# Kernel tuning notes

Hardware: AMD Instinct MI355X
Metric: run time of the kernel (lower is better)

Reference implementation:

```python
import jax, jax.numpy as jnp
import numpy as np

NUM_LAYERS, D_IN, D_M, D_S, D_D, K = 4, 768, 1536, 16, 96, 4
EPS = 1e-6


def rmsnorm(x, w):
    return x * jax.lax.rsqrt(jnp.mean(x * x, axis=-1, keepdims=True) + EPS) * w


def depthwise_causal_conv(x, w, b):
    # x: [B, D_M, L], w: [D_M, K], b: [D_M]
    # torch Conv1d with padding=K-1 followed by [..., :L] == causal left-pad conv
    xp = jnp.pad(x, ((0, 0), (0, 0), (K - 1, 0)))
    y = jax.lax.conv_general_dilated(
        xp, w[:, None, :], (1,), 'VALID',
        dimension_numbers=('NCH', 'OIH', 'NCH'),
        feature_group_count=D_M)
    return y + b[None, :, None]


def mamba_block(seq, in_w, out_w, sB, sC, sD0, sD1w, sD1b, cw, cb, A_log, Dp):
    ab = seq @ in_w.T                       # [B,L,2*D_M]
    a, bgate = ab[..., :D_M], ab[..., D_M:]
    x = jnp.swapaxes(a, 1, 2)               # [B,D_M,L]
    a = jnp.swapaxes(depthwise_causal_conv(x, cw, cb), 1, 2)
    a = jax.nn.silu(a)
    # --- selective SSM ---
    A = -jnp.exp(A_log)                     # [D_M,D_S]
    Bm = a @ sB.T                           # [B,L,D_S]
    Cm = a @ sC.T                           # [B,L,D_S]
    delta = jax.nn.softplus((a @ sD0.T) @ sD1w.T + sD1b)  # [B,L,D_M]
    A_bar = jnp.exp(delta[..., None] * A)   # [B,L,D_M,D_S]
    X_bar = delta[..., None] * Bm[:, :, None, :] * a[..., None]

    def step(h, AX):
        At, Xt = AX                         # [B,D_M,D_S]
        h = At * h + Xt
        return h, h

    h0 = jnp.zeros((seq.shape[0], D_M, D_S), seq.dtype)
    _, hs = jax.lax.scan(step, h0, (jnp.swapaxes(A_bar, 0, 1), jnp.swapaxes(X_bar, 0, 1)))
    hid = jnp.swapaxes(hs, 0, 1)            # [B,L,D_M,D_S]
    out = jnp.einsum('blds,bls->bld', hid, Cm) + Dp * a
    out = out * jax.nn.silu(bgate)
    return out @ out_w.T


def setup_inputs() -> dict:
    key = jax.random.key(0)
    ks = jax.random.split(key, 16)
    s = 0.02
    tok = jax.random.randint(ks[0], (2, 1024), 0, 32000)
    embedding = jax.random.normal(ks[1], (32000, D_IN), jnp.float32) * s
    in_proj_w = jax.random.normal(ks[2], (NUM_LAYERS, 2 * D_M, D_IN), jnp.float32) * (D_IN ** -0.5)
    out_proj_w = jax.random.normal(ks[3], (NUM_LAYERS, D_IN, D_M), jnp.float32) * (D_M ** -0.5)
    sB_w = jax.random.normal(ks[4], (NUM_LAYERS, D_S, D_M), jnp.float32) * (D_M ** -0.5)
    sC_w = jax.random.normal(ks[5], (NUM_LAYERS, D_S, D_M), jnp.float32) * (D_M ** -0.5)
    sD0_w = jax.random.normal(ks[6], (NUM_LAYERS, D_D, D_M), jnp.float32) * (D_M ** -0.5)
    sD1_w = jax.random.uniform(ks[7], (NUM_LAYERS, D_M, D_D), jnp.float32, -(D_D ** -0.5), D_D ** -0.5)
    # dt-bias init exactly as in the module
    u = jax.random.uniform(ks[8], (NUM_LAYERS, D_M), jnp.float32)
    dt = jnp.clip(jnp.exp(u * (np.log(0.1) - np.log(0.001)) + np.log(0.001)), 1e-4, None)
    sD1_b = dt + jnp.log(-jnp.expm1(-dt))
    conv_w = jax.random.normal(ks[9], (NUM_LAYERS, D_M, K), jnp.float32) * (K ** -0.5)
    conv_b = jnp.zeros((NUM_LAYERS, D_M), jnp.float32)
    A_log = jnp.broadcast_to(jnp.log(jnp.arange(1, D_S + 1, dtype=jnp.float32)), (NUM_LAYERS, D_M, D_S))
    D = jnp.ones((NUM_LAYERS, D_M), jnp.float32)
    norm_w = jnp.ones((NUM_LAYERS, D_IN), jnp.float32)
    norm_f_w = jnp.ones((D_IN,), jnp.float32)
    head_w = jax.random.normal(ks[10], (32000, D_IN), jnp.float32) * (D_IN ** -0.5)
    return dict(tok=tok, embedding=embedding, in_proj_w=in_proj_w, out_proj_w=out_proj_w,
                sB_w=sB_w, sC_w=sC_w, sD0_w=sD0_w, sD1_w=sD1_w, sD1_b=sD1_b,
                conv_w=conv_w, conv_b=conv_b, A_log=A_log, D=D,
                norm_w=norm_w, norm_f_w=norm_f_w, head_w=head_w)


def reference(tok, embedding, in_proj_w, out_proj_w, sB_w, sC_w, sD0_w, sD1_w, sD1_b,
              conv_w, conv_b, A_log, D, norm_w, norm_f_w, head_w):
    seq = embedding[tok]                    # [B,L,D_IN]
    for i in range(NUM_LAYERS):
        seq = mamba_block(rmsnorm(seq, norm_w[i]),
                          in_proj_w[i], out_proj_w[i], sB_w[i], sC_w[i],
                          sD0_w[i], sD1_w[i], sD1_b[i], conv_w[i], conv_b[i],
                          A_log[i], D[i]) + seq
    seq = rmsnorm(seq, norm_f_w)
    return seq @ head_w.T                   # [B,L,vocab]
```

## Files before the change

kernel.cpp:

```cpp
#include <hip/hip_runtime.h>
#include <math.h>

#define BATCH 2
#define SEQLEN 1024
#define NTOK 2048
#define DIN 768
#define DM 1536
#define DS 16
#define DD 96
#define EPS 1e-6f
#define NC 64
#define CL 16
#define NG (BATCH*DM*DS)

typedef __attribute__((ext_vector_type(8))) short short8;
typedef __attribute__((ext_vector_type(4))) float f32x4;

static __device__ __forceinline__ unsigned short f2bf(float f) {
    unsigned int u = __float_as_uint(f);
    u += 0x7fff + ((u >> 16) & 1);
    return (unsigned short)(u >> 16);
}

__global__ __launch_bounds__(192) void embed_kernel(const int* __restrict__ tok,
                                                    const float* __restrict__ emb,
                                                    float* __restrict__ seq) {
    int m = blockIdx.x;
    int t = tok[m];
    const float4* src = (const float4*)(emb + (size_t)t * DIN);
    float4* dst = (float4*)(seq + (size_t)m * DIN);
    dst[threadIdx.x] = src[threadIdx.x];
}

__global__ __launch_bounds__(256) void zero_kernel(float* __restrict__ p, int n4) {
    int i = blockIdx.x * 256 + threadIdx.x;
    if (i < n4) ((float4*)p)[i] = make_float4(0.f, 0.f, 0.f, 0.f);
}

__global__ __launch_bounds__(256) void wcat_kernel(const float* __restrict__ sB,
                                                   const float* __restrict__ sC,
                                                   const float* __restrict__ sD0,
                                                   unsigned short* __restrict__ out) {
    int idx = blockIdx.x * 256 + threadIdx.x;
    int k = idx % DM;
    int row = (idx / DM) & 127;
    int layer = idx / (DM * 128);
    float v;
    if (row < 16)      v = sB[((size_t)layer * 16 + row) * DM + k];
    else if (row < 32) v = sC[((size_t)layer * 16 + (row - 16)) * DM + k];
    else               v = sD0[((size_t)layer * 96 + (row - 32)) * DM + k];
    out[idx] = f2bf(v);
}

__global__ __launch_bounds__(256) void rmsnorm_kernel(const float* __restrict__ in,
                                                      const float* __restrict__ w,
                                                      unsigned short* __restrict__ out) {
    int m = blockIdx.x;
    const float* x = in + (size_t)m * DIN;
    float v[3];
    float s = 0.f;
#pragma unroll
    for (int j = 0; j < 3; j++) {
        v[j] = x[threadIdx.x + 256 * j];
        s += v[j] * v[j];
    }
#pragma unroll
    for (int off = 32; off; off >>= 1) s += __shfl_down(s, off);
    __shared__ float wsum[4];
    int lane = threadIdx.x & 63, wv = threadIdx.x >> 6;
    if (lane == 0) wsum[wv] = s;
    __syncthreads();
    float tot = wsum[0] + wsum[1] + wsum[2] + wsum[3];
    float scale = rsqrtf(tot / (float)DIN + EPS);
#pragma unroll
    for (int j = 0; j < 3; j++) {
        int c = threadIdx.x + 256 * j;
        out[(size_t)m * DIN + c] = f2bf(v[j] * scale * w[c]);
    }
}

template <int EPI, int BSRC, int KSPLIT, int XCDSWZ>
__global__ __launch_bounds__(256) void gemm_mfma(const unsigned short* __restrict__ A,
                                                 const void* __restrict__ Bv,
                                                 float* __restrict__ C, int N, int K, int nbx) {
    __shared__ unsigned short As[128 * 32];
    __shared__ unsigned short Bs[128 * 32];
    int tid = threadIdx.x;
    int lane = tid & 63, w = tid >> 6;
    int wm = w >> 1, wn = w & 1;
    int fm = lane & 15, fk = lane >> 4;

    int bx, by;
    if (XCDSWZ) {
        int lin = blockIdx.y * gridDim.x + blockIdx.x;
        int q = gridDim.x >> 3;
        int x = lin & 7;
        int t = lin >> 3;
        by = t % gridDim.y;
        bx = x * q + t / gridDim.y;
        if (bx >= nbx) return;
    } else {
        bx = blockIdx.x; by = blockIdx.y;
    }

    const unsigned short* Ab   = A + (size_t)by * 128 * K;
    const unsigned short* Bb16 = (const unsigned short*)Bv + (size_t)bx * 128 * K;
    const float*          Bb32 = (const float*)Bv + (size_t)bx * 128 * K;
    int r0 = tid >> 2;
    int ko = (tid & 3) * 8;
    const float* Bp = Bb32 + (size_t)(tid >> 1) * K + (tid & 1) * 16;

    int kchunk = K / KSPLIT;
    int kbeg = (KSPLIT > 1) ? blockIdx.z * kchunk : 0;
    int kend = kbeg + kchunk;

    f32x4 acc[4][4];
#pragma unroll
    for (int i = 0; i < 4; i++)
#pragma unroll
        for (int j = 0; j < 4; j++) acc[i][j] = (f32x4){0.f, 0.f, 0.f, 0.f};

    float4 bc0, bc1, bc2, bc3;
    unsigned short *bdst0 = nullptr, *bdst1 = nullptr;
    if (BSRC == 1) {
        int r = tid >> 1;
        int sz = (r >> 1) & 3;
        int d0 = (tid & 1) * 2;
        bdst0 = Bs + r * 32 + ((d0 + 0) ^ sz) * 8;
        bdst1 = Bs + r * 32 + ((d0 + 1) ^ sz) * 8;
        bc0 = *(const float4*)(Bp + kbeg);
        bc1 = *(const float4*)(Bp + kbeg + 4);
        bc2 = *(const float4*)(Bp + kbeg + 8);
        bc3 = *(const float4*)(Bp + kbeg + 12);
    }

    for (int k0 = kbeg; k0 < kend; k0 += 32) {
        __syncthreads();
        if (BSRC == 1) {
            short8 p0, p1;
            p0[0] = (short)f2bf(bc0.x); p0[1] = (short)f2bf(bc0.y);
            p0[2] = (short)f2bf(bc0.z); p0[3] = (short)f2bf(bc0.w);
            p0[4] = (short)f2bf(bc1.x); p0[5] = (short)f2bf(bc1.y);
            p0[6] = (short)f2bf(bc1.z); p0[7] = (short)f2bf(bc1.w);
            p1[0] = (short)f2bf(bc2.x); p1[1] = (short)f2bf(bc2.y);
            p1[2] = (short)f2bf(bc2.z); p1[3] = (short)f2bf(bc2.w);
            p1[4] = (short)f2bf(bc3.x); p1[5] = (short)f2bf(bc3.y);
            p1[6] = (short)f2bf(bc3.z); p1[7] = (short)f2bf(bc3.w);
            *(short8*)bdst0 = p0;
            *(short8*)bdst1 = p1;
        }
#pragma unroll
        for (int j = 0; j < 2; j++) {
            int row = r0 + j * 64;
            int c = tid + j * 256;
            __builtin_amdgcn_global_load_lds(
                (const __attribute__((address_space(1))) unsigned int*)(const void*)(Ab + (size_t)row * K + k0 + ko),
                (__attribute__((address_space(3))) unsigned int*)(void*)(As + c * 8), 16, 0, 0);
            if (BSRC == 0)
                __builtin_amdgcn_global_load_lds(
                    (const __attribute__((address_space(1))) unsigned int*)(const void*)(Bb16 + (size_t)row * K + k0 + ko),
                    (__attribute__((address_space(3))) unsigned int*)(void*)(Bs + c * 8), 16, 0, 0);
        }
        __syncthreads();

        if (BSRC == 1) {
            int kn = (k0 + 32 < kend) ? (k0 + 32) : kbeg;
            bc0 = *(const float4*)(Bp + kn);
            bc1 = *(const float4*)(Bp + kn + 4);
            bc2 = *(const float4*)(Bp + kn + 8);
            bc3 = *(const float4*)(Bp + kn + 12);
        }

        short8 af[4], bfv[4];
#pragma unroll
        for (int i = 0; i < 4; i++)
            af[i] = *(const short8*)(As + (wm * 64 + i * 16 + fm) * 32 + fk * 8);
#pragma unroll
        for (int j = 0; j < 4; j++) {
            int R = wn * 64 + j * 16 + fm;
            int dswz = (BSRC == 1) ? (fk ^ ((R >> 1) & 3)) : fk;
            bfv[j] = *(const short8*)(Bs + R * 32 + dswz * 8);
        }
#pragma unroll
        for (int i = 0; i < 4; i++)
#pragma unroll
            for (int j = 0; j < 4; j++)
                acc[i][j] = __builtin_amdgcn_mfma_f32_16x16x32_bf16(af[i], bfv[j], acc[i][j], 0, 0, 0);
    }

    int rowb = by * 128 + wm * 64;
    int colb = bx * 128 + wn * 64;
#pragma unroll
    for (int i = 0; i < 4; i++)
#pragma unroll
        for (int j = 0; j < 4; j++)
#pragma unroll
            for (int r = 0; r < 4; r++) {
                int row = rowb + i * 16 + fk * 4 + r;
                int col = colb + j * 16 + fm;
                size_t off = (size_t)row * N + col;
                if (EPI == 0)      C[off] = acc[i][j][r];
                else if (EPI == 1) C[off] += acc[i][j][r];
                else               unsafeAtomicAdd(&C[off], acc[i][j][r]);
            }
}

__global__ __launch_bounds__(256) void conv_silu_kernel(const float* __restrict__ ab,
                                                        const float* __restrict__ cw,
                                                        const float* __restrict__ cb,
                                                        float* __restrict__ out,
                                                        unsigned short* __restrict__ outb) {
    int idx = blockIdx.x * 256 + threadIdx.x;
    int c = idx % DM;
    int t = idx / DM;
    int l = t % SEQLEN;
    float4 w4 = ((const float4*)cw)[c];
    float y = cb[c];
    y = fmaf(w4.w, ab[(size_t)t * (2 * DM) + c], y);
    if (l >= 1) y = fmaf(w4.z, ab[(size_t)(t - 1) * (2 * DM) + c], y);
    if (l >= 2) y = fmaf(w4.y, ab[(size_t)(t - 2) * (2 * DM) + c], y);
    if (l >= 3) y = fmaf(w4.x, ab[(size_t)(t - 3) * (2 * DM) + c], y);
    float sv = y / (1.f + expf(-y));
    out[(size_t)t * DM + c] = sv;
    outb[(size_t)t * DM + c] = f2bf(sv);
}

__global__ __launch_bounds__(256) void gemm32_softplus(const float* __restrict__ A, int lda,
                                                       const float* __restrict__ B,
                                                       float* __restrict__ C, int N, int K,
                                                       const float* __restrict__ bias) {
    __shared__ float As[16][68];
    __shared__ float Bs[16][68];
    int tid = threadIdx.x;
    int lr = tid >> 2;
    int lk = (tid & 3) << 2;
    const float* Aptr = A + (size_t)(blockIdx.y * 64 + lr) * lda + lk;
    const float* Bptr = B + (size_t)(blockIdx.x * 64 + lr) * K + lk;
    int tx = tid & 15, ty = tid >> 4;
    float acc[4][4] = {};
    for (int k0 = 0; k0 < K; k0 += 16) {
        float4 av = *(const float4*)(Aptr + k0);
        float4 bv = *(const float4*)(Bptr + k0);
        __syncthreads();
        As[lk + 0][lr] = av.x; As[lk + 1][lr] = av.y;
        As[lk + 2][lr] = av.z; As[lk + 3][lr] = av.w;
        Bs[lk + 0][lr] = bv.x; Bs[lk + 1][lr] = bv.y;
        Bs[lk + 2][lr] = bv.z; Bs[lk + 3][lr] = bv.w;
        __syncthreads();
#pragma unroll
        for (int kk = 0; kk < 16; kk++) {
            float4 a4 = *(const float4*)&As[kk][ty * 4];
            float4 b4 = *(const float4*)&Bs[kk][tx * 4];
            float aa[4] = {a4.x, a4.y, a4.z, a4.w};
            float bb[4] = {b4.x, b4.y, b4.z, b4.w};
#pragma unroll
            for (int i = 0; i < 4; i++)
#pragma unroll
                for (int j = 0; j < 4; j++)
                    acc[i][j] = fmaf(aa[i], bb[j], acc[i][j]);
        }
    }
    int row0 = blockIdx.y * 64 + ty * 4;
    int col0 = blockIdx.x * 64 + tx * 4;
    float4 bsv = *(const float4*)(bias + col0);
    float bb[4] = {bsv.x, bsv.y, bsv.z, bsv.w};
#pragma unroll
    for (int i = 0; i < 4; i++) {
        float* cp = C + (size_t)(row0 + i) * N + col0;
        float r[4];
#pragma unroll
        for (int j = 0; j < 4; j++) {
            float xv = acc[i][j] + bb[j];
            r[j] = fmaxf(xv, 0.f) + log1pf(expf(-fabsf(xv)));
        }
        *(float4*)cp = make_float4(r[0], r[1], r[2], r[3]);
    }
}

__global__ __launch_bounds__(256) void scan_chunk(const float* __restrict__ delta,
                                                  const float* __restrict__ a,
                                                  const float* __restrict__ bcd,
                                                  const float* __restrict__ A_log,
                                                  float* __restrict__ P, float* __restrict__ S) {
    int tid = threadIdx.x;
    int blk = blockIdx.x;
    int dblk = blk % (DM / 256);
    int c = (blk / (DM / 256)) % NC;
    int b = blk / ((DM / 256) * NC);
    int d = dblk * 256 + tid;
    int t0 = b * SEQLEN + c * CL;

    __shared__ float LB[CL][16];
    {
        int row = tid >> 4, col = tid & 15;
        LB[row][col] = bcd[(size_t)(t0 + row) * 128 + col];
    }
    __syncthreads();

    float An[16];
    {
        const float4* ap = (const float4*)(A_log + (size_t)d * 16);
#pragma unroll
        for (int q = 0; q < 4; q++) {
            float4 v = ap[q];
            An[q * 4 + 0] = -expf(v.x); An[q * 4 + 1] = -expf(v.y);
            An[q * 4 + 2] = -expf(v.z); An[q * 4 + 3] = -expf(v.w);
        }
    }
    float h[16], Pv[16];
#pragma unroll
    for (int s = 0; s < 16; s++) { h[s] = 0.f; Pv[s] = 1.f; }

    for (int l = 0; l < CL; l++) {
        int t = t0 + l;
        float dv = delta[(size_t)t * DM + d];
        float av = a[(size_t)t * DM + d];
        float dva = dv * av;
#pragma unroll
        for (int s = 0; s < 16; s++) {
            float e = expf(dv * An[s]);
            Pv[s] *= e;
            h[s] = fmaf(e, h[s], dva * LB[l][s]);
        }
    }
    size_t g0 = (size_t)c * NG + (size_t)(b * DM + d) * 16;
#pragma unroll
    for (int q = 0; q < 4; q++) {
        *(f32x4*)(P + g0 + q * 4) = (f32x4){Pv[q*4], Pv[q*4+1], Pv[q*4+2], Pv[q*4+3]};
        *(f32x4*)(S + g0 + q * 4) = (f32x4){h[q*4], h[q*4+1], h[q*4+2], h[q*4+3]};
    }
}

__global__ __launch_bounds__(256) void scan_combine(const float* __restrict__ P,
                                                    const float* __restrict__ S,
                                                    float* __restrict__ Hb) {
    int g = blockIdx.x * 256 + threadIdx.x;
    float h = 0.f;
#pragma unroll
    for (int c = 0; c < NC; c++) {
        Hb[c * NG + g] = h;
        h = P[c * NG + g] * h + S[c * NG + g];
    }
}

__global__ __launch_bounds__(256) void scan_apply(const float* __restrict__ delta,
                                                  const float* __restrict__ a,
                                                  const float* __restrict__ bcd,
                                                  const float* __restrict__ ab,
                                                  const float* __restrict__ A_log,
                                                  const float* __restrict__ Dp,
                                                  const float* __restrict__ Hb,
                                                  float* __restrict__ y1,
                                                  unsigned short* __restrict__ y1b) {
    int tid = threadIdx.x;
    int blk = blockIdx.x;
    int dblk = blk % (DM / 256);
    int c = (blk / (DM / 256)) % NC;
    int b = blk / ((DM / 256) * NC);
    int d = dblk * 256 + tid;
    int t0 = b * SEQLEN + c * CL;

    __shared__ float LB[CL][32];
    {
        int row = tid >> 4, col = (tid & 15) * 2;
        *(float2*)&LB[row][col] = *(const float2*)&bcd[(size_t)(t0 + row) * 128 + col];
    }
    __syncthreads();

    float An[16];
    {
        const float4* ap = (const float4*)(A_log + (size_t)d * 16);
#pragma unroll
        for (int q = 0; q < 4; q++) {
            float4 v = ap[q];
            An[q * 4 + 0] = -expf(v.x); An[q * 4 + 1] = -expf(v.y);
            An[q * 4 + 2] = -expf(v.z); An[q * 4 + 3] = -expf(v.w);
        }
    }
    float Dv = Dp[d];
    float h[16];
    {
        const float* hp = Hb + (size_t)c * NG + (size_t)(b * DM + d) * 16;
#pragma unroll
        for (int q = 0; q < 4; q++) {
            float4 v = *(const float4*)(hp + q * 4);
            h[q * 4 + 0] = v.x; h[q * 4 + 1] = v.y; h[q * 4 + 2] = v.z; h[q * 4 + 3] = v.w;
        }
    }

    for (int l = 0; l < CL; l++) {
        int t = t0 + l;
        float dv = delta[(size_t)t * DM + d];
        float av = a[(size_t)t * DM + d];
        float dva = dv * av;
        float ct = 0.f;
#pragma unroll
        for (int s = 0; s < 16; s++) {
            float e = expf(dv * An[s]);
            h[s] = fmaf(e, h[s], dva * LB[l][s]);
            ct = fmaf(h[s], LB[l][16 + s], ct);
        }
        float bg = ab[(size_t)t * 2 * DM + DM + d];
        float sl = bg / (1.f + expf(-bg));
        float y = (ct + Dv * av) * sl;
        y1[(size_t)t * DM + d] = y;
        y1b[(size_t)t * DM + d] = f2bf(y);
    }
}

extern "C" void kernel_launch(void* const* d_in, const int* in_sizes, int n_in,
                              void* d_out, int out_size, void* d_ws, size_t ws_size,
                              hipStream_t stream) {
    const int* tok        = (const int*)d_in[0];
    const float* emb      = (const float*)d_in[1];
    const float* in_proj  = (const float*)d_in[2];
    const float* out_proj = (const float*)d_in[3];
    const float* sB       = (const float*)d_in[4];
    const float* sC       = (const float*)d_in[5];
    const float* sD0      = (const float*)d_in[6];
    const float* sD1      = (const float*)d_in[7];
    const float* sD1b     = (const float*)d_in[8];
    const float* cw       = (const float*)d_in[9];
    const float* cb       = (const float*)d_in[10];
    const float* A_log    = (const float*)d_in[11];
    const float* Dp       = (const float*)d_in[12];
    const float* norm_w   = (const float*)d_in[13];
    const float* norm_f   = (const float*)d_in[14];
    const float* head_w   = (const float*)d_in[15];
    float* out = (float*)d_out;

    char* base = (char*)d_ws;
    float* seq   = (float*)base;          base += (size_t)NTOK * DIN * 4;
    float* ab    = (float*)base;          base += (size_t)NTOK * 2 * DM * 4;
    float* ac    = (float*)base;          base += (size_t)NTOK * DM * 4;
    float* delta = (float*)base;          base += (size_t)NTOK * DM * 4;
    float* y1    = (float*)base;          base += (size_t)NTOK * DM * 4;
    float* bcd   = (float*)base;          base += (size_t)NTOK * 128 * 4;
    unsigned short* xnb  = (unsigned short*)base;  base += (size_t)NTOK * DIN * 2;
    unsigned short* acb  = (unsigned short*)base;  base += (size_t)NTOK * DM * 2;
    unsigned short* y1b  = (unsigned short*)base;  base += (size_t)NTOK * DM * 2;
    float* P  = (float*)base;             base += (size_t)NG * NC * 4;
    float* S  = (float*)base;             base += (size_t)NG * NC * 4;
    float* Hb = (float*)base;             base += (size_t)NG * NC * 4;
    unsigned short* wcatb = (unsigned short*)base; base += (size_t)4 * 128 * DM * 2;

    embed_kernel<<<NTOK, 192, 0, stream>>>(tok, emb, seq);
    wcat_kernel<<<4 * 128 * DM / 256, 256, 0, stream>>>(sB, sC, sD0, wcatb);

    for (int i = 0; i < 4; i++) {
        rmsnorm_kernel<<<NTOK, 256, 0, stream>>>(seq, norm_w + i * DIN, xnb);
        gemm_mfma<0, 1, 1, 1><<<dim3(2 * DM / 128, NTOK / 128), 256, 0, stream>>>(
            xnb, in_proj + (size_t)i * 2 * DM * DIN, ab, 2 * DM, DIN, 2 * DM / 128);
        conv_silu_kernel<<<NTOK * DM / 256, 256, 0, stream>>>(
            ab, cw + (size_t)i * DM * 4, cb + (size_t)i * DM, ac, acb);
        zero_kernel<<<NTOK * 128 / 4 / 256, 256, 0, stream>>>(bcd, NTOK * 128 / 4);
        gemm_mfma<2, 0, 4, 0><<<dim3(1, NTOK / 128, 4), 256, 0, stream>>>(
            acb, wcatb + (size_t)i * 128 * DM, bcd, 128, DM, 1);
        gemm32_softplus<<<dim3(DM / 64, NTOK / 64), 256, 0, stream>>>(
            bcd + 32, 128, sD1 + (size_t)i * DM * DD, delta, DM, DD, sD1b + (size_t)i * DM);
        scan_chunk<<<BATCH * NC * (DM / 256), 256, 0, stream>>>(
            delta, ac, bcd, A_log + (size_t)i * DM * DS, P, S);
        scan_combine<<<NG / 256, 256, 0, stream>>>(P, S, Hb);
        scan_apply<<<BATCH * NC * (DM / 256), 256, 0, stream>>>(
            delta, ac, bcd, ab, A_log + (size_t)i * DM * DS, Dp + (size_t)i * DM, Hb, y1, y1b);
        gemm_mfma<2, 1, 2, 0><<<dim3(DIN / 128, NTOK / 128, 2), 256, 0, stream>>>(
            y1b, out_proj + (size_t)i * DIN * DM, seq, DIN, DM, DIN / 128);
    }
    rmsnorm_kernel<<<NTOK, 256, 0, stream>>>(seq, norm_f, xnb);
    gemm_mfma<0, 1, 1, 1><<<dim3(256, NTOK / 128), 256, 0, stream>>>(
        xnb, head_w, out, 32000, DIN, 32000 / 128);
}
```

Before: 1.465 ms.

## Pre-cast GEMM weights to bf16 and deepen MFMA K-tile to 64 with swizzle

Adds a cast kernel that converts in_proj, out_proj and head weights to bf16 up front, so every GEMM loads both operands through direct global-to-LDS copies instead of converting fp32 inside the main loop. The GEMM K-tile grows from 32 to 64 with an XOR swizzle on LDS rows. Split-K factors for the small GEMMs are raised, and the unused fp32 y1 output is dropped. The buffers are aliased (Hb onto P, head bf16 onto ab), and the up-front casts add extra traffic on every call.

```diff
diff --git a/kernel.cpp b/kernel.cpp
--- a/kernel.cpp
+++ b/kernel.cpp
@@ -35,6 +35,17 @@
 __global__ __launch_bounds__(256) void zero_kernel(float* __restrict__ p, int n4) {
     int i = blockIdx.x * 256 + threadIdx.x;
     if (i < n4) ((float4*)p)[i] = make_float4(0.f, 0.f, 0.f, 0.f);
+}
+
+__global__ __launch_bounds__(256) void cast_kernel(const float* __restrict__ in,
+                                                   unsigned short* __restrict__ out, int n4) {
+    int i = blockIdx.x * 256 + threadIdx.x;
+    if (i < n4) {
+        float4 v = ((const float4*)in)[i];
+        ushort4 r;
+        r.x = f2bf(v.x); r.y = f2bf(v.y); r.z = f2bf(v.z); r.w = f2bf(v.w);
+        ((ushort4*)out)[i] = r;
+    }
 }
 
 __global__ __launch_bounds__(256) void wcat_kernel(const float* __restrict__ sB,
@@ -79,12 +90,12 @@
     }
 }
 
-template <int EPI, int BSRC, int KSPLIT, int XCDSWZ>
+template <int EPI, int KSPLIT, int XCDSWZ>
 __global__ __launch_bounds__(256) void gemm_mfma(const unsigned short* __restrict__ A,
-                                                 const void* __restrict__ Bv,
+                                                 const unsigned short* __restrict__ B,
                                                  float* __restrict__ C, int N, int K, int nbx) {
-    __shared__ unsigned short As[128 * 32];
-    __shared__ unsigned short Bs[128 * 32];
+    __shared__ unsigned short As[128 * 64];
+    __shared__ unsigned short Bs[128 * 64];
     int tid = threadIdx.x;
     int lane = tid & 63, w = tid >> 6;
     int wm = w >> 1, wn = w & 1;
@@ -103,89 +114,63 @@
         bx = blockIdx.x; by = blockIdx.y;
     }
 
-    const unsigned short* Ab   = A + (size_t)by * 128 * K;
-    const unsigned short* Bb16 = (const unsigned short*)Bv + (size_t)bx * 128 * K;
-    const float*          Bb32 = (const float*)Bv + (size_t)bx * 128 * K;
-    int r0 = tid >> 2;
-    int ko = (tid & 3) * 8;
-    const float* Bp = Bb32 + (size_t)(tid >> 1) * K + (tid & 1) * 16;
+    const unsigned short* Ab = A + (size_t)by * 128 * K;
+    const unsigned short* Bb = B + (size_t)bx * 128 * K;
 
     int kchunk = K / KSPLIT;
     int kbeg = (KSPLIT > 1) ? blockIdx.z * kchunk : 0;
     int kend = kbeg + kchunk;
 
+    int sr[4], so[4];
+#pragma unroll
+    for (int j = 0; j < 4; j++) {
+        int c = tid + j * 256;
+        int r = c >> 3;
+        sr[j] = r;
+        so[j] = ((c ^ r) & 7) * 8;
+    }
+
     f32x4 acc[4][4];
 #pragma unroll
     for (int i = 0; i < 4; i++)
 #pragma unroll
         for (int j = 0; j < 4; j++) acc[i][j] = (f32x4){0.f, 0.f, 0.f, 0.f};
 
-    float4 bc0, bc1, bc2, bc3;
-    unsigned short *bdst0 = nullptr, *bdst1 = nullptr;
-    if (BSRC == 1) {
-        int r = tid >> 1;
-        int sz = (r >> 1) & 3;
-        int d0 = (tid & 1) * 2;
-        bdst0 = Bs + r * 32 + ((d0 + 0) ^ sz) * 8;
-        bdst1 = Bs + r * 32 + ((d0 + 1) ^ sz) * 8;
-        bc0 = *(const float4*)(Bp + kbeg);
-        bc1 = *(const float4*)(Bp + kbeg + 4);
-        bc2 = *(const float4*)(Bp + kbeg + 8);
-        bc3 = *(const float4*)(Bp + kbeg + 12);
-    }
-
-    for (int k0 = kbeg; k0 < kend; k0 += 32) {
+    for (int k0 = kbeg; k0 < kend; k0 += 64) {
         __syncthreads();
-        if (BSRC == 1) {
-            short8 p0, p1;
-            p0[0] = (short)f2bf(bc0.x); p0[1] = (short)f2bf(bc0.y);
-            p0[2] = (short)f2bf(bc0.z); p0[3] = (short)f2bf(bc0.w);
-            p0[4] = (short)f2bf(bc1.x); p0[5] = (short)f2bf(bc1.y);
-            p0[6] = (short)f2bf(bc1.z); p0[7] = (short)f2bf(bc1.w);
-            p1[0] = (short)f2bf(bc2.x); p1[1] = (short)f2bf(bc2.y);
-            p1[2] = (short)f2bf(bc2.z); p1[3] = (short)f2bf(bc2.w);
-            p1[4] = (short)f2bf(bc3.x); p1[5] = (short)f2bf(bc3.y);
-            p1[6] = (short)f2bf(bc3.z); p1[7] = (short)f2bf(bc3.w);
-            *(short8*)bdst0 = p0;
-            *(short8*)bdst1 = p1;
-        }
-#pragma unroll
-        for (int j = 0; j < 2; j++) {
-            int row = r0 + j * 64;
+#pragma unroll
+        for (int j = 0; j < 4; j++) {
             int c = tid + j * 256;
             __builtin_amdgcn_global_load_lds(
-                (const __attribute__((address_space(1))) unsigned int*)(const void*)(Ab + (size_t)row * K + k0 + ko),
+                (const __attribute__((address_space(1))) unsigned int*)(const void*)(Ab + (size_t)sr[j] * K + k0 + so[j]),
                 (__attribute__((address_space(3))) unsigned int*)(void*)(As + c * 8), 16, 0, 0);
-            if (BSRC == 0)
-                __builtin_amdgcn_global_load_lds(
-                    (const __attribute__((address_space(1))) unsigned int*)(const void*)(Bb16 + (size_t)row * K + k0 + ko),
-                    (__attribute__((address_space(3))) unsigned int*)(void*)(Bs + c * 8), 16, 0, 0);
+            __builtin_amdgcn_global_load_lds(
+                (const __attribute__((address_space(1))) unsigned int*)(const void*)(Bb + (size_t)sr[j] * K + k0 + so[j]),
+                (__attribute__((address_space(3))) unsigned int*)(void*)(Bs + c * 8), 16, 0, 0);
         }
         __syncthreads();
 
-        if (BSRC == 1) {
-            int kn = (k0 + 32 < kend) ? (k0 + 32) : kbeg;
-            bc0 = *(const float4*)(Bp + kn);
-            bc1 = *(const float4*)(Bp + kn + 4);
-            bc2 = *(const float4*)(Bp + kn + 8);
-            bc3 = *(const float4*)(Bp + kn + 12);
-        }
-
-        short8 af[4], bfv[4];
-#pragma unroll
-        for (int i = 0; i < 4; i++)
-            af[i] = *(const short8*)(As + (wm * 64 + i * 16 + fm) * 32 + fk * 8);
-#pragma unroll
-        for (int j = 0; j < 4; j++) {
-            int R = wn * 64 + j * 16 + fm;
-            int dswz = (BSRC == 1) ? (fk ^ ((R >> 1) & 3)) : fk;
-            bfv[j] = *(const short8*)(Bs + R * 32 + dswz * 8);
-        }
-#pragma unroll
-        for (int i = 0; i < 4; i++)
-#pragma unroll
-            for (int j = 0; j < 4; j++)
-                acc[i][j] = __builtin_amdgcn_mfma_f32_16x16x32_bf16(af[i], bfv[j], acc[i][j], 0, 0, 0);
+#pragma unroll
+        for (int kk = 0; kk < 2; kk++) {
+            short8 af[4], bfv[4];
+#pragma unroll
+            for (int i = 0; i < 4; i++) {
+                int R = wm * 64 + i * 16 + fm;
+                int dsw = (kk * 4 + fk) ^ (R & 7);
+                af[i] = *(const short8*)(As + R * 64 + dsw * 8);
+            }
+#pragma unroll
+            for (int j = 0; j < 4; j++) {
+                int R = wn * 64 + j * 16 + fm;
+                int dsw = (kk * 4 + fk) ^ (R & 7);
+                bfv[j] = *(const short8*)(Bs + R * 64 + dsw * 8);
+            }
+#pragma unroll
+            for (int i = 0; i < 4; i++)
+#pragma unroll
+                for (int j = 0; j < 4; j++)
+                    acc[i][j] = __builtin_amdgcn_mfma_f32_16x16x32_bf16(af[i], bfv[j], acc[i][j], 0, 0, 0);
+        }
     }
 
     int rowb = by * 128 + wm * 64;
@@ -338,8 +323,10 @@
     float h = 0.f;
 #pragma unroll
     for (int c = 0; c < NC; c++) {
+        float Pv = P[c * NG + g];
+        float Sv = S[c * NG + g];
         Hb[c * NG + g] = h;
-        h = P[c * NG + g] * h + S[c * NG + g];
+        h = fmaf(Pv, h, Sv);
     }
 }
 
@@ -350,7 +337,6 @@
                                                   const float* __restrict__ A_log,
                                                   const float* __restrict__ Dp,
                                                   const float* __restrict__ Hb,
-                                                  float* __restrict__ y1,
                                                   unsigned short* __restrict__ y1b) {
     int tid = threadIdx.x;
     int blk = blockIdx.x;
@@ -403,7 +389,6 @@
         float bg = ab[(size_t)t * 2 * DM + DM + d];
         float sl = bg / (1.f + expf(-bg));
         float y = (ct + Dv * av) * sl;
-        y1[(size_t)t * DM + d] = y;
         y1b[(size_t)t * DM + d] = f2bf(y);
     }
 }
@@ -434,27 +419,31 @@
     float* ab    = (float*)base;          base += (size_t)NTOK * 2 * DM * 4;
     float* ac    = (float*)base;          base += (size_t)NTOK * DM * 4;
     float* delta = (float*)base;          base += (size_t)NTOK * DM * 4;
-    float* y1    = (float*)base;          base += (size_t)NTOK * DM * 4;
     float* bcd   = (float*)base;          base += (size_t)NTOK * 128 * 4;
     unsigned short* xnb  = (unsigned short*)base;  base += (size_t)NTOK * DIN * 2;
     unsigned short* acb  = (unsigned short*)base;  base += (size_t)NTOK * DM * 2;
     unsigned short* y1b  = (unsigned short*)base;  base += (size_t)NTOK * DM * 2;
     float* P  = (float*)base;             base += (size_t)NG * NC * 4;
     float* S  = (float*)base;             base += (size_t)NG * NC * 4;
-    float* Hb = (float*)base;             base += (size_t)NG * NC * 4;
+    unsigned short* inpb  = (unsigned short*)base; base += (size_t)4 * 2 * DM * DIN * 2;
+    unsigned short* outpb = (unsigned short*)base; base += (size_t)4 * DIN * DM * 2;
     unsigned short* wcatb = (unsigned short*)base; base += (size_t)4 * 128 * DM * 2;
+    float* Hb = P;
+    unsigned short* headb = (unsigned short*)ab;
 
     embed_kernel<<<NTOK, 192, 0, stream>>>(tok, emb, seq);
     wcat_kernel<<<4 * 128 * DM / 256, 256, 0, stream>>>(sB, sC, sD0, wcatb);
+    cast_kernel<<<(4 * 2 * DM * DIN / 4 + 255) / 256, 256, 0, stream>>>(in_proj, inpb, 4 * 2 * DM * DIN / 4);
+    cast_kernel<<<(4 * DIN * DM / 4 + 255) / 256, 256, 0, stream>>>(out_proj, outpb, 4 * DIN * DM / 4);
 
     for (int i = 0; i < 4; i++) {
         rmsnorm_kernel<<<NTOK, 256, 0, stream>>>(seq, norm_w + i * DIN, xnb);
-        gemm_mfma<0, 1, 1, 1><<<dim3(2 * DM / 128, NTOK / 128), 256, 0, stream>>>(
-            xnb, in_proj + (size_t)i * 2 * DM * DIN, ab, 2 * DM, DIN, 2 * DM / 128);
+        gemm_mfma<0, 1, 1><<<dim3(2 * DM / 128, NTOK / 128), 256, 0, stream>>>(
+            xnb, inpb + (size_t)i * 2 * DM * DIN, ab, 2 * DM, DIN, 2 * DM / 128);
         conv_silu_kernel<<<NTOK * DM / 256, 256, 0, stream>>>(
             ab, cw + (size_t)i * DM * 4, cb + (size_t)i * DM, ac, acb);
         zero_kernel<<<NTOK * 128 / 4 / 256, 256, 0, stream>>>(bcd, NTOK * 128 / 4);
-        gemm_mfma<2, 0, 4, 0><<<dim3(1, NTOK / 128, 4), 256, 0, stream>>>(
+        gemm_mfma<2, 8, 0><<<dim3(1, NTOK / 128, 8), 256, 0, stream>>>(
             acb, wcatb + (size_t)i * 128 * DM, bcd, 128, DM, 1);
         gemm32_softplus<<<dim3(DM / 64, NTOK / 64), 256, 0, stream>>>(
             bcd + 32, 128, sD1 + (size_t)i * DM * DD, delta, DM, DD, sD1b + (size_t)i * DM);
@@ -462,11 +451,12 @@
             delta, ac, bcd, A_log + (size_t)i * DM * DS, P, S);
         scan_combine<<<NG / 256, 256, 0, stream>>>(P, S, Hb);
         scan_apply<<<BATCH * NC * (DM / 256), 256, 0, stream>>>(
-            delta, ac, bcd, ab, A_log + (size_t)i * DM * DS, Dp + (size_t)i * DM, Hb, y1, y1b);
-        gemm_mfma<2, 1, 2, 0><<<dim3(DIN / 128, NTOK / 128, 2), 256, 0, stream>>>(
-            y1b, out_proj + (size_t)i * DIN * DM, seq, DIN, DM, DIN / 128);
+            delta, ac, bcd, ab, A_log + (size_t)i * DM * DS, Dp + (size_t)i * DM, Hb, y1b);
+        gemm_mfma<2, 4, 0><<<dim3(DIN / 128, NTOK / 128, 4), 256, 0, stream>>>(
+            y1b, outpb + (size_t)i * DIN * DM, seq, DIN, DM, DIN / 128);
     }
     rmsnorm_kernel<<<NTOK, 256, 0, stream>>>(seq, norm_f, xnb);
-    gemm_mfma<0, 1, 1, 1><<<dim3(256, NTOK / 128), 256, 0, stream>>>(
-        xnb, head_w, out, 32000, DIN, 32000 / 128);
-}
+    cast_kernel<<<(32000 * DIN / 4 + 255) / 256, 256, 0, stream>>>(head_w, headb, 32000 * DIN / 4);
+    gemm_mfma<0, 1, 1><<<dim3(256, NTOK / 128), 256, 0, stream>>>(
+        xnb, headb, out, 32000, DIN, 32000 / 128);
+}
```

Result: faster. 1.309 ms (-10.6%).
